# Kernel tuning notes

Measured on AMD Instinct MI355X. Metric: run time of the kernel, lower is better.

The kernel has to match this reference:

```python
import jax, jax.numpy as jnp
import numpy as np

LN_EPS = 1e-5
DEG_EPS = 1e-12


def setup_inputs() -> dict:
    key = jax.random.key(0)
    k1, k2, k3, k4 = jax.random.split(key, 4)
    N, E, D = 100000, 1000000, 64
    x = jax.random.normal(k1, (N, D), dtype=jnp.float32)
    edge_index = jax.random.randint(k2, (2, E), 0, N, dtype=jnp.int64)
    edge_weight = jax.random.uniform(k3, (E,), dtype=jnp.float32)
    # xavier_uniform for Linear(D, D): bound = sqrt(6/(D+D))
    bound = float(np.sqrt(6.0 / (D + D)))
    W = jax.random.uniform(k4, (D, D), dtype=jnp.float32, minval=-bound, maxval=bound)
    b = jnp.zeros((D,), dtype=jnp.float32)
    ln_gamma = jnp.ones((D,), dtype=jnp.float32)
    ln_beta = jnp.zeros((D,), dtype=jnp.float32)
    return {"x": x, "edge_index": edge_index, "edge_weight": edge_weight,
            "W": W, "b": b, "ln_gamma": ln_gamma, "ln_beta": ln_beta}


def reference(x, edge_index, edge_weight, W, b, ln_gamma, ln_beta):
    N = x.shape[0]
    # --- add self loops with weight 1.0 ---
    diag = jnp.arange(N, dtype=edge_index.dtype)
    ei = jnp.concatenate([edge_index, jnp.stack([diag, diag], axis=0)], axis=1)
    ew = jnp.concatenate([edge_weight.astype(jnp.float32),
                          jnp.ones((N,), dtype=jnp.float32)], axis=0)
    row, col = ei[0], ei[1]
    # --- renormalized adjacency weights: D^{-1/2}(A+I)D^{-1/2} ---
    deg = jax.ops.segment_sum(ew, row, num_segments=N)  # [N]
    deg_inv_sqrt = (deg + DEG_EPS) ** -0.5
    nw = ew * deg_inv_sqrt[row] * deg_inv_sqrt[col]     # [E+N]
    # --- SpMM: gather, scale, segment-sum ---
    msg = x[col] * nw[:, None].astype(x.dtype)          # [E+N, D]
    h = jax.ops.segment_sum(msg, row, num_segments=N)   # [N, D]
    # --- linear + gelu (exact erf) + layernorm + residual ---
    y = h @ W.T + b
    y = jax.nn.gelu(y, approximate=False)
    mean = jnp.mean(y, axis=-1, keepdims=True)
    var = jnp.mean(jnp.square(y - mean), axis=-1, keepdims=True)
    y = (y - mean) * jax.lax.rsqrt(var + LN_EPS) * ln_gamma + ln_beta
    return y + x
```

## Files before the change

kernel.cpp:

```cpp
#include <hip/hip_runtime.h>
#include <math.h>

#define DEG_EPS 1e-12f
#define LN_EPS  1e-5f
#define BROWS   256
#define CAPA    3072
#define MAXBKT  512

typedef __attribute__((ext_vector_type(8))) short bf16x8;
typedef __attribute__((ext_vector_type(4))) float f32x4;

__device__ __forceinline__ short f2bf(float f) {
    unsigned u = __float_as_uint(f);
    u += 0x7FFF + ((u >> 16) & 1);
    return (short)(u >> 16);
}
__device__ __forceinline__ float bf_lo(unsigned u) { return __uint_as_float(u << 16); }
__device__ __forceinline__ float bf_hi(unsigned u) { return __uint_as_float(u & 0xFFFF0000u); }


__global__ __launch_bounds__(256) void k_prep(
    const int* __restrict__ rows, const int* __restrict__ cols,
    const float* __restrict__ ew,
    int* __restrict__ bktcnt, int2* __restrict__ bktbuf,
    const float* __restrict__ x, const float* __restrict__ W,
    unsigned short* __restrict__ xwb,
    int E, int N, int NBKT, int Ntiles, int cB)
{
    const int tid = threadIdx.x;
    if ((int)blockIdx.x < cB) {
        __shared__ int hist[MAXBKT];
        __shared__ int base_s[MAXBKT];
        __shared__ int cur[MAXBKT];
        int per = (E + cB - 1) / cB;
        int e0 = blockIdx.x * per;
        int e1 = e0 + per; if (e1 > E) e1 = E;
        for (int t0 = e0; t0 < e1; t0 += 4096) {
            int tc = e1 - t0; if (tc > 4096) tc = 4096;
            for (int i = tid; i < NBKT; i += 256) { hist[i] = 0; cur[i] = 0; }
            __syncthreads();
            for (int i = t0 + tid; i < t0 + tc; i += 256)
                atomicAdd(&hist[rows[i] >> 8], 1);
            __syncthreads();
            for (int i = tid; i < NBKT; i += 256) {
                int h = hist[i];
                base_s[i] = h ? atomicAdd(&bktcnt[i], h) : 0;
            }
            __syncthreads();
            for (int i = t0 + tid; i < t0 + tc; i += 256) {
                int r = rows[i];
                int bkt = r >> 8;
                int slot = base_s[bkt] + atomicAdd(&cur[bkt], 1);
                if (slot < CAPA)
                    bktbuf[(size_t)bkt * CAPA + slot] =
                        make_int2(((r & 255) << 17) | cols[i], __float_as_int(ew[i]));
            }
            __syncthreads();
        }
    } else {
        const int lane = tid & 63;
        const int m = lane & 15;
        const int q = lane >> 4;
        const int xwB = gridDim.x - cB;
        const int wave = (blockIdx.x - cB) * 4 + (tid >> 6);
        const int nwv = xwB * 4;

        bf16x8 bfrag[4][2];
#pragma unroll
        for (int f = 0; f < 4; ++f)
#pragma unroll
            for (int s = 0; s < 2; ++s) {
                const float4* wp = (const float4*)(W + (f * 16 + m) * 64 + s * 32 + q * 8);
                float4 lo = wp[0], hi = wp[1];
                bf16x8 v;
                v[0] = f2bf(lo.x); v[1] = f2bf(lo.y); v[2] = f2bf(lo.z); v[3] = f2bf(lo.w);
                v[4] = f2bf(hi.x); v[5] = f2bf(hi.y); v[6] = f2bf(hi.z); v[7] = f2bf(hi.w);
                bfrag[f][s] = v;
            }

        for (int t = wave; t < Ntiles; t += nwv) {
            int n0 = t * 16;
            int nr = n0 + m; if (nr >= N) nr = N - 1;
            bf16x8 afrag[2];
#pragma unroll
            for (int s = 0; s < 2; ++s) {
                const float4* xp = (const float4*)(x + (size_t)nr * 64 + s * 32 + q * 8);
                float4 lo = xp[0], hi = xp[1];
                bf16x8 v;
                v[0] = f2bf(lo.x); v[1] = f2bf(lo.y); v[2] = f2bf(lo.z); v[3] = f2bf(lo.w);
                v[4] = f2bf(hi.x); v[5] = f2bf(hi.y); v[6] = f2bf(hi.z); v[7] = f2bf(hi.w);
                afrag[s] = v;
            }
#pragma unroll
            for (int f = 0; f < 4; ++f) {
                f32x4 acc = {0.f, 0.f, 0.f, 0.f};
                acc = __builtin_amdgcn_mfma_f32_16x16x32_bf16(afrag[0], bfrag[f][0], acc, 0, 0, 0);
                acc = __builtin_amdgcn_mfma_f32_16x16x32_bf16(afrag[1], bfrag[f][1], acc, 0, 0, 0);
#pragma unroll
                for (int r4 = 0; r4 < 4; ++r4) {
                    int node = n0 + q * 4 + r4;
                    if (node < N)
                        xwb[(size_t)node * 64 + f * 16 + m] = (unsigned short)f2bf(acc[r4]);
                }
            }
        }
    }
}

__global__ __launch_bounds__(256) void k_build(
    const int* __restrict__ bktcnt, const int2* __restrict__ bktbuf,
    int2* __restrict__ meta, int2* __restrict__ rowinfo, float* __restrict__ dis,
    int N)
{
    __shared__ int      cnt[256];
    __shared__ unsigned sum[256];
    __shared__ int      off[256];
    __shared__ int      cur[256];
    __shared__ int      sc[256];
    const int bkt = blockIdx.x, t = threadIdx.x;
    cnt[t] = 0; sum[t] = 0; cur[t] = 0;
    __syncthreads();

    int nb = bktcnt[bkt];
    if (nb > CAPA) nb = CAPA;
    const int2* buf = bktbuf + (size_t)bkt * CAPA;

    for (int i = t; i < nb; i += 256) {
        int2 e = buf[i];
        int rlo = (e.x >> 17) & 255;
        atomicAdd(&cnt[rlo], 1);
        atomicAdd(&sum[rlo], __float2uint_rn(__int_as_float(e.y) * 16777216.0f));
    }
    __syncthreads();

    int v = cnt[t]; sc[t] = v; __syncthreads();
    for (int o = 1; o < 256; o <<= 1) {
        int u = (t >= o) ? sc[t - o] : 0;
        __syncthreads();
        sc[t] += u;
        __syncthreads();
    }
    off[t] = sc[t] - v;

    const int mbase = bkt * CAPA;
    int r = bkt * 256 + t;
    if (r < N) {
        rowinfo[r] = make_int2(mbase + off[t], v);
        float deg = 1.0f + (float)sum[t] * (1.0f / 16777216.0f);
        dis[r] = rsqrtf(deg + DEG_EPS);
    }
    __syncthreads();

    for (int i = t; i < nb; i += 256) {
        int2 e = buf[i];
        int rlo = (e.x >> 17) & 255;
        int o = atomicAdd(&cur[rlo], 1);
        meta[mbase + off[rlo] + o] = make_int2(e.x & 0x1FFFF, e.y);
    }
}

__global__ __launch_bounds__(256) void k_spmm_fused(
    const int2* __restrict__ rowinfo, const int2* __restrict__ meta,
    const float* __restrict__ dis, const uint2* __restrict__ xw4,
    const float* __restrict__ x, const float* __restrict__ bias,
    const float* __restrict__ gamma, const float* __restrict__ beta,
    float* __restrict__ out, int N)
{
    int t = blockIdx.x * blockDim.x + threadIdx.x;
    int row = t >> 6;
    if (row >= N) return;
    const int lane = t & 63;
    const int k  = lane & 15;
    const int qh = lane >> 4;

    int2 ri = rowinfo[row];
    int start = ri.x;
    int cnt = ri.y < 64 ? ri.y : 64;
    float s = dis[row];

    float a0 = 0.f, a1 = 0.f, a2 = 0.f, a3 = 0.f;
    if (qh == 0) {
        float s2 = s * s;
        uint2 v = xw4[(size_t)row * 16 + k];
        a0 = bf_lo(v.x) * s2; a1 = bf_hi(v.x) * s2;
        a2 = bf_lo(v.y) * s2; a3 = bf_hi(v.y) * s2;
    }

    int c = 0; float w = 0.f;
    if (lane < cnt) {
        int2 m = meta[start + lane];
        c = m.x;
        w = __int_as_float(m.y) * s * dis[c];
    }

    int tmax = (cnt + 3) >> 2;
    int tt = 0;
    for (; tt + 2 <= tmax; tt += 2) {
        int j0 = 4 * tt + qh, j1 = j0 + 4;
        int   c0 = __shfl(c, j0, 64);
        float w0 = __shfl(w, j0, 64);
        int   c1 = __shfl(c, j1, 64);
        float w1 = __shfl(w, j1, 64);
        uint2 v0 = xw4[(size_t)c0 * 16 + k];
        uint2 v1 = xw4[(size_t)c1 * 16 + k];
        a0 = fmaf(bf_lo(v0.x), w0, a0); a1 = fmaf(bf_hi(v0.x), w0, a1);
        a2 = fmaf(bf_lo(v0.y), w0, a2); a3 = fmaf(bf_hi(v0.y), w0, a3);
        a0 = fmaf(bf_lo(v1.x), w1, a0); a1 = fmaf(bf_hi(v1.x), w1, a1);
        a2 = fmaf(bf_lo(v1.y), w1, a2); a3 = fmaf(bf_hi(v1.y), w1, a3);
    }
    if (tt < tmax) {
        int j = 4 * tt + qh;
        int   cc = __shfl(c, j, 64);
        float ww = __shfl(w, j, 64);
        uint2 v = xw4[(size_t)cc * 16 + k];
        a0 = fmaf(bf_lo(v.x), ww, a0); a1 = fmaf(bf_hi(v.x), ww, a1);
        a2 = fmaf(bf_lo(v.y), ww, a2); a3 = fmaf(bf_hi(v.y), ww, a3);
    }

#pragma unroll
    for (int mk = 16; mk < 64; mk <<= 1) {
        a0 += __shfl_xor(a0, mk, 64);
        a1 += __shfl_xor(a1, mk, 64);
        a2 += __shfl_xor(a2, mk, 64);
        a3 += __shfl_xor(a3, mk, 64);
    }

    float a = (qh == 0) ? a0 : (qh == 1) ? a1 : (qh == 2) ? a2 : a3;
    int f = 4 * k + qh;
    a += bias[f];
    a = 0.5f * a * (1.0f + erff(a * 0.70710678118654752f));

    float sum = a, ssq = a * a;
#pragma unroll
    for (int mk = 1; mk < 64; mk <<= 1) {
        sum += __shfl_xor(sum, mk, 64);
        ssq += __shfl_xor(ssq, mk, 64);
    }
    float mean = sum * (1.0f / 64.0f);
    float var  = fmaxf(ssq * (1.0f / 64.0f) - mean * mean, 0.0f);
    float rs   = rsqrtf(var + LN_EPS);
    float nrm  = (a - mean) * rs;

    float nv = __shfl(nrm, ((lane & 3) << 4) | (lane >> 2), 64);
    out[(size_t)row * 64 + lane] =
        nv * gamma[lane] + beta[lane] + x[(size_t)row * 64 + lane];
}

extern "C" void kernel_launch(void* const* d_in, const int* in_sizes, int n_in,
                              void* d_out, int out_size, void* d_ws, size_t ws_size,
                              hipStream_t stream) {
    const float* x   = (const float*)d_in[0];
    const int*   ei  = (const int*)  d_in[1];
    const float* ew  = (const float*)d_in[2];
    const float* W   = (const float*)d_in[3];
    const float* b   = (const float*)d_in[4];
    const float* g   = (const float*)d_in[5];
    const float* bt  = (const float*)d_in[6];
    float* out = (float*)d_out;

    const int N = in_sizes[0] / 64;
    const int E = in_sizes[1] / 2;
    const int* rows = ei;
    const int* cols = ei + E;
    const int Ntiles = (N + 15) / 16;
    const int NBKT = (N + BROWS - 1) / BROWS;

    char* w8 = (char*)d_ws;
    int2*  bktbuf = (int2*)w8;                    w8 += (size_t)NBKT * CAPA * 8;
    int2*  meta   = (int2*)w8;                    w8 += (size_t)NBKT * CAPA * 8;
    int2*  rowinfo= (int2*)w8;                    w8 += (size_t)N * 8;
    unsigned short* xwb = (unsigned short*)w8;    w8 += (size_t)N * 128;
    float* dis    = (float*)w8;                   w8 += (size_t)N * 4;
    int*   bktcnt = (int*)w8;

    hipMemsetAsync(bktcnt, 0, (size_t)NBKT * 4, stream);

    const int cB = 256, xB = 768;
    k_prep<<<cB + xB, 256, 0, stream>>>(rows, cols, ew, bktcnt, bktbuf,
                                        x, W, xwb, E, N, NBKT, Ntiles, cB);

    k_build<<<NBKT, 256, 0, stream>>>(bktcnt, bktbuf, meta, rowinfo, dis, N);

    long total = (long)N * 64;
    k_spmm_fused<<<(int)((total + 255) / 256), 256, 0, stream>>>(
        rowinfo, meta, dis, (const uint2*)xwb, x, b, g, bt, out, N);
}
```

Measured before the change: 168.9 us.

## Fuse per-row edge sorting into SpMM kernel via shared-memory bucketing

Removes the global meta and rowinfo sort output. k_build becomes a small degree-only kernel, and each SpMM block rescans its bucket, counting and scattering the edges of its 64 rows into shared memory with precomputed normalized weights. This saves a global write and re-read of the sorted edge list. The cost is that every bucket is now read four times (once per quad block), and edges are dropped if a quad exceeds SCAP=1024. The prep kernel's grid sizes are also doubled.

```diff
diff --git a/kernel.cpp b/kernel.cpp
--- a/kernel.cpp
+++ b/kernel.cpp
@@ -6,6 +6,7 @@
 #define BROWS   256
 #define CAPA    3072
 #define MAXBKT  512
+#define SCAP    1024
 
 typedef __attribute__((ext_vector_type(8))) short bf16x8;
 typedef __attribute__((ext_vector_type(4))) float f32x4;
@@ -107,143 +108,165 @@
     }
 }
 
-__global__ __launch_bounds__(256) void k_build(
+__global__ __launch_bounds__(256) void k_dis(
     const int* __restrict__ bktcnt, const int2* __restrict__ bktbuf,
-    int2* __restrict__ meta, int2* __restrict__ rowinfo, float* __restrict__ dis,
-    int N)
+    float* __restrict__ dis, int N)
 {
-    __shared__ int      cnt[256];
-    __shared__ unsigned sum[256];
-    __shared__ int      off[256];
-    __shared__ int      cur[256];
-    __shared__ int      sc[256];
+    __shared__ unsigned lsum[256];
     const int bkt = blockIdx.x, t = threadIdx.x;
-    cnt[t] = 0; sum[t] = 0; cur[t] = 0;
-    __syncthreads();
-
+    lsum[t] = 0;
+    __syncthreads();
     int nb = bktcnt[bkt];
     if (nb > CAPA) nb = CAPA;
     const int2* buf = bktbuf + (size_t)bkt * CAPA;
-
     for (int i = t; i < nb; i += 256) {
         int2 e = buf[i];
-        int rlo = (e.x >> 17) & 255;
-        atomicAdd(&cnt[rlo], 1);
-        atomicAdd(&sum[rlo], __float2uint_rn(__int_as_float(e.y) * 16777216.0f));
-    }
-    __syncthreads();
-
-    int v = cnt[t]; sc[t] = v; __syncthreads();
-    for (int o = 1; o < 256; o <<= 1) {
-        int u = (t >= o) ? sc[t - o] : 0;
-        __syncthreads();
-        sc[t] += u;
-        __syncthreads();
-    }
-    off[t] = sc[t] - v;
-
-    const int mbase = bkt * CAPA;
-    int r = bkt * 256 + t;
+        atomicAdd(&lsum[(e.x >> 17) & 255],
+                  __float2uint_rn(__int_as_float(e.y) * 16777216.0f));
+    }
+    __syncthreads();
+    int r = bkt * BROWS + t;
     if (r < N) {
-        rowinfo[r] = make_int2(mbase + off[t], v);
-        float deg = 1.0f + (float)sum[t] * (1.0f / 16777216.0f);
+        float deg = 1.0f + (float)lsum[t] * (1.0f / 16777216.0f);
         dis[r] = rsqrtf(deg + DEG_EPS);
     }
-    __syncthreads();
-
-    for (int i = t; i < nb; i += 256) {
-        int2 e = buf[i];
-        int rlo = (e.x >> 17) & 255;
-        int o = atomicAdd(&cur[rlo], 1);
-        meta[mbase + off[rlo] + o] = make_int2(e.x & 0x1FFFF, e.y);
-    }
 }
 
 __global__ __launch_bounds__(256) void k_spmm_fused(
-    const int2* __restrict__ rowinfo, const int2* __restrict__ meta,
+    const int* __restrict__ bktcnt, const int2* __restrict__ bktbuf,
     const float* __restrict__ dis, const uint2* __restrict__ xw4,
     const float* __restrict__ x, const float* __restrict__ bias,
     const float* __restrict__ gamma, const float* __restrict__ beta,
     float* __restrict__ out, int N)
 {
-    int t = blockIdx.x * blockDim.x + threadIdx.x;
-    int row = t >> 6;
-    if (row >= N) return;
-    const int lane = t & 63;
+    __shared__ int2  srt[SCAP];
+    __shared__ int   cnt[64], off[64], cur[64], sc[64];
+    __shared__ float sdis[64];
+    const int t = threadIdx.x;
+    const int bkt = blockIdx.x >> 2, quad = blockIdx.x & 3;
+    const int r0 = bkt * BROWS + quad * 64;
+
+    if (t < 64) {
+        cnt[t] = 0; cur[t] = 0;
+        sdis[t] = (r0 + t < N) ? dis[r0 + t] : 1.0f;
+    }
+    __syncthreads();
+
+    int nb = bktcnt[bkt];
+    if (nb > CAPA) nb = CAPA;
+    const int2* buf = bktbuf + (size_t)bkt * CAPA;
+
+    for (int i = t; i < nb; i += 256) {
+        int rq = (buf[i].x >> 17) & 255;
+        if ((rq >> 6) == quad) atomicAdd(&cnt[rq & 63], 1);
+    }
+    __syncthreads();
+    if (t < 64) sc[t] = cnt[t];
+    __syncthreads();
+    for (int o = 1; o < 64; o <<= 1) {
+        int u = 0;
+        if (t < 64 && t >= o) u = sc[t - o];
+        __syncthreads();
+        if (t < 64) sc[t] += u;
+        __syncthreads();
+    }
+    if (t < 64) off[t] = sc[t] - cnt[t];
+    __syncthreads();
+
+    for (int i = t; i < nb; i += 256) {
+        int2 e = buf[i];
+        int rq = (e.x >> 17) & 255;
+        if ((rq >> 6) == quad) {
+            int rl = rq & 63;
+            int c = e.x & 0x1FFFF;
+            float w = __int_as_float(e.y) * sdis[rl] * dis[c];
+            int pos = off[rl] + atomicAdd(&cur[rl], 1);
+            if (pos < SCAP)
+                srt[pos] = make_int2(c, __float_as_int(w));
+        }
+    }
+    __syncthreads();
+
+    const int lane = t & 63, wv = t >> 6;
     const int k  = lane & 15;
     const int qh = lane >> 4;
 
-    int2 ri = rowinfo[row];
-    int start = ri.x;
-    int cnt = ri.y < 64 ? ri.y : 64;
-    float s = dis[row];
-
-    float a0 = 0.f, a1 = 0.f, a2 = 0.f, a3 = 0.f;
-    if (qh == 0) {
-        float s2 = s * s;
-        uint2 v = xw4[(size_t)row * 16 + k];
-        a0 = bf_lo(v.x) * s2; a1 = bf_hi(v.x) * s2;
-        a2 = bf_lo(v.y) * s2; a3 = bf_hi(v.y) * s2;
-    }
-
-    int c = 0; float w = 0.f;
-    if (lane < cnt) {
-        int2 m = meta[start + lane];
-        c = m.x;
-        w = __int_as_float(m.y) * s * dis[c];
-    }
-
-    int tmax = (cnt + 3) >> 2;
-    int tt = 0;
-    for (; tt + 2 <= tmax; tt += 2) {
-        int j0 = 4 * tt + qh, j1 = j0 + 4;
-        int   c0 = __shfl(c, j0, 64);
-        float w0 = __shfl(w, j0, 64);
-        int   c1 = __shfl(c, j1, 64);
-        float w1 = __shfl(w, j1, 64);
-        uint2 v0 = xw4[(size_t)c0 * 16 + k];
-        uint2 v1 = xw4[(size_t)c1 * 16 + k];
-        a0 = fmaf(bf_lo(v0.x), w0, a0); a1 = fmaf(bf_hi(v0.x), w0, a1);
-        a2 = fmaf(bf_lo(v0.y), w0, a2); a3 = fmaf(bf_hi(v0.y), w0, a3);
-        a0 = fmaf(bf_lo(v1.x), w1, a0); a1 = fmaf(bf_hi(v1.x), w1, a1);
-        a2 = fmaf(bf_lo(v1.y), w1, a2); a3 = fmaf(bf_hi(v1.y), w1, a3);
-    }
-    if (tt < tmax) {
-        int j = 4 * tt + qh;
-        int   cc = __shfl(c, j, 64);
-        float ww = __shfl(w, j, 64);
-        uint2 v = xw4[(size_t)cc * 16 + k];
-        a0 = fmaf(bf_lo(v.x), ww, a0); a1 = fmaf(bf_hi(v.x), ww, a1);
-        a2 = fmaf(bf_lo(v.y), ww, a2); a3 = fmaf(bf_hi(v.y), ww, a3);
-    }
-
-#pragma unroll
-    for (int mk = 16; mk < 64; mk <<= 1) {
-        a0 += __shfl_xor(a0, mk, 64);
-        a1 += __shfl_xor(a1, mk, 64);
-        a2 += __shfl_xor(a2, mk, 64);
-        a3 += __shfl_xor(a3, mk, 64);
-    }
-
-    float a = (qh == 0) ? a0 : (qh == 1) ? a1 : (qh == 2) ? a2 : a3;
-    int f = 4 * k + qh;
-    a += bias[f];
-    a = 0.5f * a * (1.0f + erff(a * 0.70710678118654752f));
-
-    float sum = a, ssq = a * a;
-#pragma unroll
-    for (int mk = 1; mk < 64; mk <<= 1) {
-        sum += __shfl_xor(sum, mk, 64);
-        ssq += __shfl_xor(ssq, mk, 64);
-    }
-    float mean = sum * (1.0f / 64.0f);
-    float var  = fmaxf(ssq * (1.0f / 64.0f) - mean * mean, 0.0f);
-    float rs   = rsqrtf(var + LN_EPS);
-    float nrm  = (a - mean) * rs;
-
-    float nv = __shfl(nrm, ((lane & 3) << 4) | (lane >> 2), 64);
-    out[(size_t)row * 64 + lane] =
-        nv * gamma[lane] + beta[lane] + x[(size_t)row * 64 + lane];
+    for (int i = 0; i < 16; ++i) {
+        const int rl = wv * 16 + i;
+        const int row = r0 + rl;
+        if (row >= N) break;
+
+        int rcnt = cnt[rl]; if (rcnt > 64) rcnt = 64;
+        int rbase = off[rl];
+        float s = sdis[rl];
+
+        float a0 = 0.f, a1 = 0.f, a2 = 0.f, a3 = 0.f;
+        if (qh == 0) {
+            float s2 = s * s;
+            uint2 v = xw4[(size_t)row * 16 + k];
+            a0 = bf_lo(v.x) * s2; a1 = bf_hi(v.x) * s2;
+            a2 = bf_lo(v.y) * s2; a3 = bf_hi(v.y) * s2;
+        }
+
+        int c = 0; float w = 0.f;
+        if (lane < rcnt) {
+            int2 m = srt[rbase + lane];
+            c = m.x;
+            w = __int_as_float(m.y);
+        }
+
+        int tmax = (rcnt + 3) >> 2;
+        int tt = 0;
+        for (; tt + 2 <= tmax; tt += 2) {
+            int j0 = 4 * tt + qh, j1 = j0 + 4;
+            int   c0 = __shfl(c, j0, 64);
+            float w0 = __shfl(w, j0, 64);
+            int   c1 = __shfl(c, j1, 64);
+            float w1 = __shfl(w, j1, 64);
+            uint2 v0 = xw4[(size_t)c0 * 16 + k];
+            uint2 v1 = xw4[(size_t)c1 * 16 + k];
+            a0 = fmaf(bf_lo(v0.x), w0, a0); a1 = fmaf(bf_hi(v0.x), w0, a1);
+            a2 = fmaf(bf_lo(v0.y), w0, a2); a3 = fmaf(bf_hi(v0.y), w0, a3);
+            a0 = fmaf(bf_lo(v1.x), w1, a0); a1 = fmaf(bf_hi(v1.x), w1, a1);
+            a2 = fmaf(bf_lo(v1.y), w1, a2); a3 = fmaf(bf_hi(v1.y), w1, a3);
+        }
+        if (tt < tmax) {
+            int j = 4 * tt + qh;
+            int   cc = __shfl(c, j, 64);
+            float ww = __shfl(w, j, 64);
+            uint2 v = xw4[(size_t)cc * 16 + k];
+            a0 = fmaf(bf_lo(v.x), ww, a0); a1 = fmaf(bf_hi(v.x), ww, a1);
+            a2 = fmaf(bf_lo(v.y), ww, a2); a3 = fmaf(bf_hi(v.y), ww, a3);
+        }
+
+#pragma unroll
+        for (int mk = 16; mk < 64; mk <<= 1) {
+            a0 += __shfl_xor(a0, mk, 64);
+            a1 += __shfl_xor(a1, mk, 64);
+            a2 += __shfl_xor(a2, mk, 64);
+            a3 += __shfl_xor(a3, mk, 64);
+        }
+
+        float a = (qh == 0) ? a0 : (qh == 1) ? a1 : (qh == 2) ? a2 : a3;
+        int f = 4 * k + qh;
+        a += bias[f];
+        a = 0.5f * a * (1.0f + erff(a * 0.70710678118654752f));
+
+        float sum = a, ssq = a * a;
+#pragma unroll
+        for (int mk = 1; mk < 64; mk <<= 1) {
+            sum += __shfl_xor(sum, mk, 64);
+            ssq += __shfl_xor(ssq, mk, 64);
+        }
+        float mean = sum * (1.0f / 64.0f);
+        float var  = fmaxf(ssq * (1.0f / 64.0f) - mean * mean, 0.0f);
+        float rs   = rsqrtf(var + LN_EPS);
+        float nrm  = (a - mean) * rs;
+
+        float nv = __shfl(nrm, ((lane & 3) << 4) | (lane >> 2), 64);
+        out[(size_t)row * 64 + lane] =
+            nv * gamma[lane] + beta[lane] + x[(size_t)row * 64 + lane];
+    }
 }
 
 extern "C" void kernel_launch(void* const* d_in, const int* in_sizes, int n_in,
@@ -267,21 +290,19 @@
 
     char* w8 = (char*)d_ws;
     int2*  bktbuf = (int2*)w8;                    w8 += (size_t)NBKT * CAPA * 8;
-    int2*  meta   = (int2*)w8;                    w8 += (size_t)NBKT * CAPA * 8;
-    int2*  rowinfo= (int2*)w8;                    w8 += (size_t)N * 8;
     unsigned short* xwb = (unsigned short*)w8;    w8 += (size_t)N * 128;
     float* dis    = (float*)w8;                   w8 += (size_t)N * 4;
     int*   bktcnt = (int*)w8;
 
     hipMemsetAsync(bktcnt, 0, (size_t)NBKT * 4, stream);
 
-    const int cB = 256, xB = 768;
+    const int cB = 512, xB = 1536;
     k_prep<<<cB + xB, 256, 0, stream>>>(rows, cols, ew, bktcnt, bktbuf,
                                         x, W, xwb, E, N, NBKT, Ntiles, cB);
 
-    k_build<<<NBKT, 256, 0, stream>>>(bktcnt, bktbuf, meta, rowinfo, dis, N);
-
-    long total = (long)N * 64;
-    k_spmm_fused<<<(int)((total + 255) / 256), 256, 0, stream>>>(
-        rowinfo, meta, dis, (const uint2*)xwb, x, b, g, bt, out, N);
-}
+    k_dis<<<NBKT, 256, 0, stream>>>(bktcnt, bktbuf, dis, N);
+
+    const int qblocks = (N + 63) / 64;
+    k_spmm_fused<<<qblocks, 256, 0, stream>>>(
+        bktcnt, bktbuf, dis, (const uint2*)xwb, x, b, g, bt, out, N);
+}
```

New measurement: 182.5 us. 8.1% more time.

## Move x@W GEMM into build kernel and widen binning across more blocks

Applied to the files above, without the earlier changes.

Edge binning now runs as its own kernel with one block per 2048-edge chunk, caching row ids in shared memory instead of re-reading them. The bf16 MFMA x@W transform moves from the binning kernel into the bucket-build kernel, which holds each bucket's edges in registers rather than reading the bucket buffer twice. Blocks grow to 512 threads. The aim is to spread binning over far more blocks and overlap the GEMM with the bucket build, at the cost of more global atomics on bucket counters.

```diff
diff --git a/kernel.cpp b/kernel.cpp
--- a/kernel.cpp
+++ b/kernel.cpp
@@ -6,6 +6,7 @@
 #define BROWS   256
 #define CAPA    3072
 #define MAXBKT  512
+#define CHUNK   2048
 
 typedef __attribute__((ext_vector_type(8))) short bf16x8;
 typedef __attribute__((ext_vector_type(4))) float f32x4;
@@ -19,51 +20,115 @@
 __device__ __forceinline__ float bf_hi(unsigned u) { return __uint_as_float(u & 0xFFFF0000u); }
 
 
-__global__ __launch_bounds__(256) void k_prep(
+__global__ __launch_bounds__(512) void k_bin(
     const int* __restrict__ rows, const int* __restrict__ cols,
     const float* __restrict__ ew,
     int* __restrict__ bktcnt, int2* __restrict__ bktbuf,
+    int E, int NBKT)
+{
+    __shared__ int hist[MAXBKT];
+    __shared__ int base_s[MAXBKT];
+    __shared__ int cur[MAXBKT];
+    __shared__ int srow[CHUNK];
+    const int t = threadIdx.x;
+    const int e0 = blockIdx.x * CHUNK;
+    const int tc = min(E - e0, CHUNK);
+
+    for (int i = t; i < NBKT; i += 512) { hist[i] = 0; cur[i] = 0; }
+    __syncthreads();
+    for (int i = t; i < tc; i += 512) {
+        int r = rows[e0 + i];
+        srow[i] = r;
+        atomicAdd(&hist[r >> 8], 1);
+    }
+    __syncthreads();
+    for (int i = t; i < NBKT; i += 512) {
+        int h = hist[i];
+        base_s[i] = h ? atomicAdd(&bktcnt[i], h) : 0;
+    }
+    __syncthreads();
+    for (int i = t; i < tc; i += 512) {
+        int r = srow[i];
+        int bkt = r >> 8;
+        int slot = base_s[bkt] + atomicAdd(&cur[bkt], 1);
+        if (slot < CAPA)
+            bktbuf[(size_t)bkt * CAPA + slot] =
+                make_int2(((r & 255) << 17) | cols[e0 + i], __float_as_int(ew[e0 + i]));
+    }
+}
+
+__global__ __launch_bounds__(512) void k_build_xw(
+    const int* __restrict__ bktcnt, const int2* __restrict__ bktbuf,
+    int2* __restrict__ meta, int2* __restrict__ rowinfo, float* __restrict__ dis,
     const float* __restrict__ x, const float* __restrict__ W,
     unsigned short* __restrict__ xwb,
-    int E, int N, int NBKT, int Ntiles, int cB)
+    int N, int NBKT, int Ntiles)
 {
-    const int tid = threadIdx.x;
-    if ((int)blockIdx.x < cB) {
-        __shared__ int hist[MAXBKT];
-        __shared__ int base_s[MAXBKT];
-        __shared__ int cur[MAXBKT];
-        int per = (E + cB - 1) / cB;
-        int e0 = blockIdx.x * per;
-        int e1 = e0 + per; if (e1 > E) e1 = E;
-        for (int t0 = e0; t0 < e1; t0 += 4096) {
-            int tc = e1 - t0; if (tc > 4096) tc = 4096;
-            for (int i = tid; i < NBKT; i += 256) { hist[i] = 0; cur[i] = 0; }
+    const int t = threadIdx.x;
+    if ((int)blockIdx.x < NBKT) {
+        __shared__ int      cnt[256];
+        __shared__ unsigned sfx[256];
+        __shared__ int      off[256];
+        __shared__ int      cur[256];
+        __shared__ int      sc[256];
+        const int bkt = blockIdx.x;
+        if (t < 256) { cnt[t] = 0; sfx[t] = 0; cur[t] = 0; }
+        __syncthreads();
+
+        int nb = bktcnt[bkt];
+        if (nb > CAPA) nb = CAPA;
+        const int2* buf = bktbuf + (size_t)bkt * CAPA;
+
+        int2 eb[6];
+#pragma unroll
+        for (int u = 0; u < 6; ++u) {
+            int i = t + u * 512;
+            eb[u] = (i < nb) ? buf[i] : make_int2(-1, 0);
+        }
+#pragma unroll
+        for (int u = 0; u < 6; ++u)
+            if (eb[u].x >= 0) {
+                int rlo = (eb[u].x >> 17) & 255;
+                atomicAdd(&cnt[rlo], 1);
+                atomicAdd(&sfx[rlo], __float2uint_rn(__int_as_float(eb[u].y) * 16777216.0f));
+            }
+        __syncthreads();
+
+        int v = 0;
+        if (t < 256) { v = cnt[t]; sc[t] = v; }
+        __syncthreads();
+        for (int o = 1; o < 256; o <<= 1) {
+            int u2 = 0;
+            if (t < 256 && t >= o) u2 = sc[t - o];
             __syncthreads();
-            for (int i = t0 + tid; i < t0 + tc; i += 256)
-                atomicAdd(&hist[rows[i] >> 8], 1);
-            __syncthreads();
-            for (int i = tid; i < NBKT; i += 256) {
-                int h = hist[i];
-                base_s[i] = h ? atomicAdd(&bktcnt[i], h) : 0;
-            }
-            __syncthreads();
-            for (int i = t0 + tid; i < t0 + tc; i += 256) {
-                int r = rows[i];
-                int bkt = r >> 8;
-                int slot = base_s[bkt] + atomicAdd(&cur[bkt], 1);
-                if (slot < CAPA)
-                    bktbuf[(size_t)bkt * CAPA + slot] =
-                        make_int2(((r & 255) << 17) | cols[i], __float_as_int(ew[i]));
-            }
+            if (t < 256) sc[t] += u2;
             __syncthreads();
         }
+        const int mbase = bkt * CAPA;
+        if (t < 256) {
+            off[t] = sc[t] - v;
+            int r = bkt * BROWS + t;
+            if (r < N) {
+                rowinfo[r] = make_int2(mbase + off[t], v);
+                float deg = 1.0f + (float)sfx[t] * (1.0f / 16777216.0f);
+                dis[r] = rsqrtf(deg + DEG_EPS);
+            }
+        }
+        __syncthreads();
+#pragma unroll
+        for (int u = 0; u < 6; ++u)
+            if (eb[u].x >= 0) {
+                int rlo = (eb[u].x >> 17) & 255;
+                int pos = off[rlo] + atomicAdd(&cur[rlo], 1);
+                meta[mbase + pos] = make_int2(eb[u].x & 0x1FFFF, eb[u].y);
+            }
     } else {
-        const int lane = tid & 63;
+        const int lane = t & 63;
         const int m = lane & 15;
         const int q = lane >> 4;
-        const int xwB = gridDim.x - cB;
-        const int wave = (blockIdx.x - cB) * 4 + (tid >> 6);
-        const int nwv = xwB * 4;
+        const int xwB = gridDim.x - NBKT;
+        const int wave = (blockIdx.x - NBKT) * 8 + (t >> 6);
+        const int nwv = xwB * 8;
 
         bf16x8 bfrag[4][2];
 #pragma unroll
@@ -72,24 +137,24 @@
             for (int s = 0; s < 2; ++s) {
                 const float4* wp = (const float4*)(W + (f * 16 + m) * 64 + s * 32 + q * 8);
                 float4 lo = wp[0], hi = wp[1];
-                bf16x8 v;
-                v[0] = f2bf(lo.x); v[1] = f2bf(lo.y); v[2] = f2bf(lo.z); v[3] = f2bf(lo.w);
-                v[4] = f2bf(hi.x); v[5] = f2bf(hi.y); v[6] = f2bf(hi.z); v[7] = f2bf(hi.w);
-                bfrag[f][s] = v;
-            }
-
-        for (int t = wave; t < Ntiles; t += nwv) {
-            int n0 = t * 16;
+                bf16x8 vv;
+                vv[0] = f2bf(lo.x); vv[1] = f2bf(lo.y); vv[2] = f2bf(lo.z); vv[3] = f2bf(lo.w);
+                vv[4] = f2bf(hi.x); vv[5] = f2bf(hi.y); vv[6] = f2bf(hi.z); vv[7] = f2bf(hi.w);
+                bfrag[f][s] = vv;
+            }
+
+        for (int tt = wave; tt < Ntiles; tt += nwv) {
+            int n0 = tt * 16;
             int nr = n0 + m; if (nr >= N) nr = N - 1;
             bf16x8 afrag[2];
 #pragma unroll
             for (int s = 0; s < 2; ++s) {
                 const float4* xp = (const float4*)(x + (size_t)nr * 64 + s * 32 + q * 8);
                 float4 lo = xp[0], hi = xp[1];
-                bf16x8 v;
-                v[0] = f2bf(lo.x); v[1] = f2bf(lo.y); v[2] = f2bf(lo.z); v[3] = f2bf(lo.w);
-                v[4] = f2bf(hi.x); v[5] = f2bf(hi.y); v[6] = f2bf(hi.z); v[7] = f2bf(hi.w);
-                afrag[s] = v;
+                bf16x8 vv;
+                vv[0] = f2bf(lo.x); vv[1] = f2bf(lo.y); vv[2] = f2bf(lo.z); vv[3] = f2bf(lo.w);
+                vv[4] = f2bf(hi.x); vv[5] = f2bf(hi.y); vv[6] = f2bf(hi.z); vv[7] = f2bf(hi.w);
+                afrag[s] = vv;
             }
 #pragma unroll
             for (int f = 0; f < 4; ++f) {
@@ -104,58 +169,6 @@
                 }
             }
         }
-    }
-}
-
-__global__ __launch_bounds__(256) void k_build(
-    const int* __restrict__ bktcnt, const int2* __restrict__ bktbuf,
-    int2* __restrict__ meta, int2* __restrict__ rowinfo, float* __restrict__ dis,
-    int N)
-{
-    __shared__ int      cnt[256];
-    __shared__ unsigned sum[256];
-    __shared__ int      off[256];
-    __shared__ int      cur[256];
-    __shared__ int      sc[256];
-    const int bkt = blockIdx.x, t = threadIdx.x;
-    cnt[t] = 0; sum[t] = 0; cur[t] = 0;
-    __syncthreads();
-
-    int nb = bktcnt[bkt];
-    if (nb > CAPA) nb = CAPA;
-    const int2* buf = bktbuf + (size_t)bkt * CAPA;
-
-    for (int i = t; i < nb; i += 256) {
-        int2 e = buf[i];
-        int rlo = (e.x >> 17) & 255;
-        atomicAdd(&cnt[rlo], 1);
-        atomicAdd(&sum[rlo], __float2uint_rn(__int_as_float(e.y) * 16777216.0f));
-    }
-    __syncthreads();
-
-    int v = cnt[t]; sc[t] = v; __syncthreads();
-    for (int o = 1; o < 256; o <<= 1) {
-        int u = (t >= o) ? sc[t - o] : 0;
-        __syncthreads();
-        sc[t] += u;
-        __syncthreads();
-    }
-    off[t] = sc[t] - v;
-
-    const int mbase = bkt * CAPA;
-    int r = bkt * 256 + t;
-    if (r < N) {
-        rowinfo[r] = make_int2(mbase + off[t], v);
-        float deg = 1.0f + (float)sum[t] * (1.0f / 16777216.0f);
-        dis[r] = rsqrtf(deg + DEG_EPS);
-    }
-    __syncthreads();
-
-    for (int i = t; i < nb; i += 256) {
-        int2 e = buf[i];
-        int rlo = (e.x >> 17) & 255;
-        int o = atomicAdd(&cur[rlo], 1);
-        meta[mbase + off[rlo] + o] = make_int2(e.x & 0x1FFFF, e.y);
     }
 }
 
@@ -275,11 +288,12 @@
 
     hipMemsetAsync(bktcnt, 0, (size_t)NBKT * 4, stream);
 
-    const int cB = 256, xB = 768;
-    k_prep<<<cB + xB, 256, 0, stream>>>(rows, cols, ew, bktcnt, bktbuf,
-                                        x, W, xwb, E, N, NBKT, Ntiles, cB);
-
-    k_build<<<NBKT, 256, 0, stream>>>(bktcnt, bktbuf, meta, rowinfo, dis, N);
+    const int binB = (E + CHUNK - 1) / CHUNK;
+    k_bin<<<binB, 512, 0, stream>>>(rows, cols, ew, bktcnt, bktbuf, E, NBKT);
+
+    const int xwB = 384;
+    k_build_xw<<<NBKT + xwB, 512, 0, stream>>>(bktcnt, bktbuf, meta, rowinfo, dis,
+                                               x, W, xwb, N, NBKT, Ntiles);
 
     long total = (long)N * 64;
     k_spmm_fused<<<(int)((total + 255) / 256), 256, 0, stream>>>(
```

Result: slower. 174.1 us (+3.1%).
